# Optimization experiments

Measured on AMD Instinct MI355X. Metric: run time of the kernel, lower is better.

Reference implementation:

```python
import jax, jax.numpy as jnp
import numpy as np

GAMMA = 1.0        # softmin temperature
BANDWIDTH = 0      # 0 => no Sakoe-Chiba band (numba code only skips when 0 < bw < |i-j|)
BIG = 1e30         # finite stand-in for +inf: exp(-BIG/gamma) underflows to exactly 0 in fp32,
                   # reproducing the inf-initialized R/SigR softmin ratios without NaNs
B, N, M = 32, 512, 512


def setup_inputs() -> dict:
    k1, k2 = jax.random.split(jax.random.key(0))
    D = jax.random.uniform(k1, (B, N, M), dtype=jnp.float32)    # pairwise distances (>= 0)
    Sig = jax.random.uniform(k2, (B, N, M), dtype=jnp.float32)  # per-cell uncertainty
    return {"D": D, "Sig": Sig}


def _soft_dtw(D, Sig):
    """uDTW forward DP (compute_softdtw), vectorized over anti-diagonal wavefronts.
    Returns jnp.stack([R[:, N, M], SigR[:, N, M]]) of shape (2, B)."""
    b, n, m = D.shape
    alpha = 1.0 / GAMMA
    # Dp[i, j] == D_new[i, j] = D[i-1, j-1] with zero border (indices 0..N, 0..M)
    Dp = jnp.pad(D, ((0, 0), (1, 0), (1, 0)))
    Sp = jnp.pad(Sig, ((0, 0), (1, 0), (1, 0)))
    iarr = jnp.arange(n + 1)

    def diag(A, d):
        # A[:, i, d - i] for i = 0..N, zero where j out of [0, M]
        j = d - iarr
        vals = A[:, iarr, jnp.clip(j, 0, m)]
        return jnp.where((j >= 0) & (j <= m), vals, 0.0)

    def shift(x, fill):
        # x[:, i-1] (index i-1 along the diagonal buffer)
        return jnp.concatenate([jnp.full((b, 1), fill, x.dtype), x[:, :-1]], axis=1)

    # diagonal buffers indexed by i; diag d=0 holds R[0,0]=0, rest inf(BIG); diag d=1 all inf
    r2 = jnp.full((b, n + 1), BIG, jnp.float32).at[:, 0].set(0.0)
    r1 = jnp.full((b, n + 1), BIG, jnp.float32)
    s2 = jnp.full((b, n + 1), BIG, jnp.float32).at[:, 0].set(0.0)
    s1 = jnp.full((b, n + 1), BIG, jnp.float32)

    def step(carry, d):
        r2, r1, s2, s1 = carry  # R/SigR diagonals d-2 and d-1
        j = d - iarr
        valid = (iarr >= 1) & (j >= 1) & (j <= m)
        if BANDWIDTH > 0:
            valid = valid & (jnp.abs(iarr - j) <= BANDWIDTH)
        # softmin ratios from R neighbors: (i-1,j-1)=prev2 shifted, (i-1,j)=prev1 shifted, (i,j-1)=prev1
        rr0 = -alpha * shift(r2, BIG)
        rr1 = -alpha * shift(r1, BIG)
        rr2 = -alpha * r1
        rmax = jnp.maximum(jnp.maximum(rr0, rr1), rr2)
        e0 = jnp.exp(rr0 - rmax)
        e1 = jnp.exp(rr1 - rmax)
        e2 = jnp.exp(rr2 - rmax)
        inv = 1.0 / (e0 + e1 + e2)
        p0, p1, p2 = e0 * inv, e1 * inv, e2 * inv
        dDd, dD1, dD2 = diag(Dp, d), diag(Dp, d - 1), diag(Dp, d - 2)
        dSd, dS1, dS2 = diag(Sp, d), diag(Sp, d - 1), diag(Sp, d - 2)
        # R[i,j] = D[i-1,j-1] + softmin-weighted avg of D_new neighbors (uDTW recurrence)
        newR = jnp.where(valid, dDd + p0 * shift(dD2, 0.0) + p1 * shift(dD1, 0.0) + p2 * dD1, BIG)
        newS = jnp.where(valid, dSd + p0 * shift(dS2, 0.0) + p1 * shift(dS1, 0.0) + p2 * dS1, BIG)
        return (r1, newR, s1, newS), None

    (_, rlast, _, slast), _ = jax.lax.scan(step, (r2, r1, s2, s1), jnp.arange(2, n + m + 1))
    # last anti-diagonal d = N + M contains cell (N, M) at index i = N
    return jnp.stack([rlast[:, n], slast[:, n]])  # (2, B)


def reference(D, Sig):
    return _soft_dtw(D, Sig)
```

## Files before the change

kernel.cpp:

```cpp
#include <hip/hip_runtime.h>


constexpr int N = 512;
constexpr int M = 512;
constexpr int BATCH = 32;
constexpr int NM = N + M;
constexpr int K = 32;
constexpr int NB = 32;
constexpr int PHASES = NB + 3;
constexpr float NL2E = -1.4426950408889634f;
constexpr float NLN2 = -0.6931471805599453f;
constexpr float EPS  = 1e-30f;

__device__ __forceinline__ float lane_shr1_or(float oldv, float x) {
  return __int_as_float(__builtin_amdgcn_update_dpp(
      __float_as_int(oldv), __float_as_int(x), 0x138, 0xf, 0xf, false));
}
__device__ __forceinline__ int qclamp(int q) {
  return q < 0 ? 0 : (q > 127 ? 127 : q);
}

__global__ __launch_bounds__(256, 1)
void softdtw_fwd(const float* __restrict__ D,
                 const float* __restrict__ Sig,
                 float* __restrict__ out) {
  const int b = blockIdx.x;
  const int t = threadIdx.x;
  const int w = t >> 6;
  const float4* DrowA4 = (const float4*)(D + ((size_t)b * N + 2 * t) * M);
  const float4* DrowB4 = (const float4*)(D + ((size_t)b * N + 2 * t + 1) * M);

  __shared__ float edgeE[4][768];
  __shared__ float edgeD[4][768];
  for (int idx = t; idx < 4 * 768; idx += 256) {
    (&edgeE[0][0])[idx] = 0.f;
    (&edgeD[0][0])[idx] = 0.f;
  }

  float eSelfA = 0.f, dSelfA = 0.f;
  float eA1 = 0.f, dA1 = 0.f;
  float eN2A = (t == 0) ? 1.f : 0.f;
  float dN2A = 0.f;
  float eSelfB = 0.f, dSelfB = 0.f;

  float sgA = 0.f, sg0 = 0.f, sg1 = 0.f, sg2 = 0.f;
  if (t == 255) {
    const float* Sb = Sig + (size_t)b * N * M;
    sgA = Sb[(size_t)(N - 1) * M + (M - 1)];
    sg0 = Sb[(size_t)(N - 2) * M + (M - 2)];
    sg1 = Sb[(size_t)(N - 2) * M + (M - 1)];
    sg2 = Sb[(size_t)(N - 1) * M + (M - 2)];
  }

  const int Bl = 4 * w, Bh = 4 * w + 19;
  const bool sA2 = (t & 1) != 0;
  const bool sB2 = (t & 1) == 0;

  float4 u0,u1,u2,u3,u4,u5,u6,u7,u8;
  float4 v0,v1,v2,v3,v4,v5,v6,v7,v8;
  {
    const int qa = (32 * Bl - 2 * t) >> 2;
    u0 = DrowA4[qclamp(qa + 0)]; u1 = DrowA4[qclamp(qa + 1)];
    u2 = DrowA4[qclamp(qa + 2)]; u3 = DrowA4[qclamp(qa + 3)];
    u4 = DrowA4[qclamp(qa + 4)]; u5 = DrowA4[qclamp(qa + 5)];
    u6 = DrowA4[qclamp(qa + 6)]; u7 = DrowA4[qclamp(qa + 7)];
    u8 = DrowA4[qclamp(qa + 8)];
    const int qb = (32 * Bl - 2 * t - 1) >> 2;
    v0 = DrowB4[qclamp(qb + 0)]; v1 = DrowB4[qclamp(qb + 1)];
    v2 = DrowB4[qclamp(qb + 2)]; v3 = DrowB4[qclamp(qb + 3)];
    v4 = DrowB4[qclamp(qb + 4)]; v5 = DrowB4[qclamp(qb + 5)];
    v6 = DrowB4[qclamp(qb + 6)]; v7 = DrowB4[qclamp(qb + 7)];
    v8 = DrowB4[qclamp(qb + 8)];
  }
  __syncthreads();

  for (int p = 0; p < PHASES; ++p) {
    const int B = p - w;
    const int nB = B + 1;
    const bool dopre = (nB >= Bl) && (nB <= Bh);

    float4 pu0,pu1,pu2,pu3,pu4,pu5,pu6,pu7,pu8;
    float4 pv0,pv1,pv2,pv3,pv4,pv5,pv6,pv7,pv8;
    if (dopre) {
      const int qa = (32 * nB - 2 * t) >> 2;
      pu0 = DrowA4[qclamp(qa + 0)]; pu1 = DrowA4[qclamp(qa + 1)];
      pu2 = DrowA4[qclamp(qa + 2)]; pu3 = DrowA4[qclamp(qa + 3)];
      pu4 = DrowA4[qclamp(qa + 4)]; pu5 = DrowA4[qclamp(qa + 5)];
      pu6 = DrowA4[qclamp(qa + 6)]; pu7 = DrowA4[qclamp(qa + 7)];
      pu8 = DrowA4[qclamp(qa + 8)];
      const int qb = (32 * nB - 2 * t - 1) >> 2;
      pv0 = DrowB4[qclamp(qb + 0)]; pv1 = DrowB4[qclamp(qb + 1)];
      pv2 = DrowB4[qclamp(qb + 2)]; pv3 = DrowB4[qclamp(qb + 3)];
      pv4 = DrowB4[qclamp(qb + 4)]; pv5 = DrowB4[qclamp(qb + 5)];
      pv6 = DrowB4[qclamp(qb + 6)]; pv7 = DrowB4[qclamp(qb + 7)];
      pv8 = DrowB4[qclamp(qb + 8)];
    }

    if (B >= Bl && B <= Bh) {
      const int d0 = 2 + B * K;
      const int cA0 = 32 * B - 2 * t;

      float4 nE0,nE1,nE2,nE3,nE4,nE5,nE6,nE7;
      float4 nD0,nD1,nD2,nD3,nD4,nD5,nD6,nD7;
      if (w > 0) {
        const int ebase = 32 * B - 128 * w + 128;
        const float4* epE = (const float4*)&edgeE[w - 1][ebase];
        const float4* epD = (const float4*)&edgeD[w - 1][ebase];
        nE0 = epE[0]; nE1 = epE[1]; nE2 = epE[2]; nE3 = epE[3];
        nE4 = epE[4]; nE5 = epE[5]; nE6 = epE[6]; nE7 = epE[7];
        nD0 = epD[0]; nD1 = epD[1]; nD2 = epD[2]; nD3 = epD[3];
        nD4 = epD[4]; nD5 = epD[5]; nD6 = epD[6]; nD7 = epD[7];
      } else {
        const float4 z = make_float4(0.f, 0.f, 0.f, 0.f);
        nE0=z;nE1=z;nE2=z;nE3=z;nE4=z;nE5=z;nE6=z;nE7=z;
        nD0=z;nD1=z;nD2=z;nD3=z;nD4=z;nD5=z;nD6=z;nD7=z;
      }

      const float
        A0=u0.x, A1=u0.y, A2=u0.z, A3=u0.w,  A4=u1.x, A5=u1.y, A6=u1.z, A7=u1.w,
        A8=u2.x, A9=u2.y, A10=u2.z, A11=u2.w, A12=u3.x, A13=u3.y, A14=u3.z, A15=u3.w,
        A16=u4.x, A17=u4.y, A18=u4.z, A19=u4.w, A20=u5.x, A21=u5.y, A22=u5.z, A23=u5.w,
        A24=u6.x, A25=u6.y, A26=u6.z, A27=u6.w, A28=u7.x, A29=u7.y, A30=u7.z, A31=u7.w,
        A32=u8.x, A33=u8.y;
      const float
        F1=v0.y, F2=v0.z, F3=v0.w,  F4=v1.x, F5=v1.y, F6=v1.z, F7=v1.w,
        F8=v2.x, F9=v2.y, F10=v2.z, F11=v2.w, F12=v3.x, F13=v3.y, F14=v3.z, F15=v3.w,
        F16=v4.x, F17=v4.y, F18=v4.z, F19=v4.w, F20=v5.x, F21=v5.y, F22=v5.z, F23=v5.w,
        F24=v6.x, F25=v6.y, F26=v6.z, F27=v6.w, F28=v7.x, F29=v7.y, F30=v7.z, F31=v7.w,
        F32=v8.x, F33=v8.y, F34=v8.z;

      const float
        gA0 =sA2?A2 :A0,  gA1 =sA2?A3 :A1,  gA2 =sA2?A4 :A2,  gA3 =sA2?A5 :A3,
        gA4 =sA2?A6 :A4,  gA5 =sA2?A7 :A5,  gA6 =sA2?A8 :A6,  gA7 =sA2?A9 :A7,
        gA8 =sA2?A10:A8,  gA9 =sA2?A11:A9,  gA10=sA2?A12:A10, gA11=sA2?A13:A11,
        gA12=sA2?A14:A12, gA13=sA2?A15:A13, gA14=sA2?A16:A14, gA15=sA2?A17:A15,
        gA16=sA2?A18:A16, gA17=sA2?A19:A17, gA18=sA2?A20:A18, gA19=sA2?A21:A19,
        gA20=sA2?A22:A20, gA21=sA2?A23:A21, gA22=sA2?A24:A22, gA23=sA2?A25:A23,
        gA24=sA2?A26:A24, gA25=sA2?A27:A25, gA26=sA2?A28:A26, gA27=sA2?A29:A27,
        gA28=sA2?A30:A28, gA29=sA2?A31:A29, gA30=sA2?A32:A30, gA31=sA2?A33:A31;
      const float
        gB0 =sB2?F3 :F1,  gB1 =sB2?F4 :F2,  gB2 =sB2?F5 :F3,  gB3 =sB2?F6 :F4,
        gB4 =sB2?F7 :F5,  gB5 =sB2?F8 :F6,  gB6 =sB2?F9 :F7,  gB7 =sB2?F10:F8,
        gB8 =sB2?F11:F9,  gB9 =sB2?F12:F10, gB10=sB2?F13:F11, gB11=sB2?F14:F12,
        gB12=sB2?F15:F13, gB13=sB2?F16:F14, gB14=sB2?F17:F15, gB15=sB2?F18:F16,
        gB16=sB2?F19:F17, gB17=sB2?F20:F18, gB18=sB2?F21:F19, gB19=sB2?F22:F20,
        gB20=sB2?F23:F21, gB21=sB2?F24:F22, gB22=sB2?F25:F23, gB23=sB2?F26:F24,
        gB24=sB2?F27:F25, gB25=sB2?F28:F26, gB26=sB2?F29:F27, gB27=sB2?F30:F28,
        gB28=sB2?F31:F29, gB29=sB2?F32:F30, gB30=sB2?F33:F31, gB31=sB2?F34:F32;

      float* pE = &edgeE[w][128 + cA0 - 1];
      float* pD = &edgeD[w][128 + cA0 - 1];

#define STEP(kk, NEv, NDv, GA, GB)                                            \
      {                                                                       \
        const float eA0v = eSelfA, dA0v = dSelfA;                             \
        const float eB0v = eSelfB, dB0v = dSelfB;                             \
        const int cA = cA0 + (kk);                                            \
        const float ddLA = (GA) * NL2E;                                       \
        const float ddLAm = ((unsigned)cA < 512u) ? ddLA : -1e30f;            \
        const float ddLB = (GB) * NL2E;                                       \
        const float ddLBm = ((unsigned)(cA - 1) < 512u) ? ddLB : -1e30f;      \
        const float sEA = lane_shr1_or((NEv), eB0v);                          \
        const float sDA = lane_shr1_or((NDv), dB0v);                          \
        const float sumA = ((eN2A + eA0v) + EPS) + sEA;                       \
        const float invA = __builtin_amdgcn_rcpf(sumA);                       \
        const float numA = fmaf(eN2A, dN2A, fmaf(sEA, sDA, eA0v * dA0v));     \
        const float rrA = fmaf(invA, numA, ddLAm);                            \
        const float newEA = __builtin_amdgcn_exp2f(rrA);                      \
        const float sumB = ((eA1 + eB0v) + EPS) + eA0v;                       \
        const float invB = __builtin_amdgcn_rcpf(sumB);                       \
        const float numB = fmaf(eA1, dA1, fmaf(eA0v, dA0v, eB0v * dB0v));     \
        const float rrB = fmaf(invB, numB, ddLBm);                            \
        const float newEB = __builtin_amdgcn_exp2f(rrB);                      \
        if (d0 + (kk) == NM && t == 255) {                                    \
          out[b] = rrB * NLN2;                                                \
          out[BATCH + b] = sgA + invB * (eA1 * sg0 + eA0v * sg1 + eB0v * sg2);\
        }                                                                     \
        eN2A = sEA; dN2A = sDA;                                               \
        eA1 = eA0v; dA1 = dA0v;                                               \
        eSelfA = newEA; dSelfA = ddLA;                                        \
        eSelfB = newEB; dSelfB = ddLB;                                        \
        pE[kk] = newEB;                                                       \
        pD[kk] = ddLB;                                                        \
      }

      STEP(0,  nE0.x, nD0.x, gA0,  gB0)
      STEP(1,  nE0.y, nD0.y, gA1,  gB1)
      STEP(2,  nE0.z, nD0.z, gA2,  gB2)
      STEP(3,  nE0.w, nD0.w, gA3,  gB3)
      STEP(4,  nE1.x, nD1.x, gA4,  gB4)
      STEP(5,  nE1.y, nD1.y, gA5,  gB5)
      STEP(6,  nE1.z, nD1.z, gA6,  gB6)
      STEP(7,  nE1.w, nD1.w, gA7,  gB7)
      STEP(8,  nE2.x, nD2.x, gA8,  gB8)
      STEP(9,  nE2.y, nD2.y, gA9,  gB9)
      STEP(10, nE2.z, nD2.z, gA10, gB10)
      STEP(11, nE2.w, nD2.w, gA11, gB11)
      STEP(12, nE3.x, nD3.x, gA12, gB12)
      STEP(13, nE3.y, nD3.y, gA13, gB13)
      STEP(14, nE3.z, nD3.z, gA14, gB14)
      STEP(15, nE3.w, nD3.w, gA15, gB15)
      STEP(16, nE4.x, nD4.x, gA16, gB16)
      STEP(17, nE4.y, nD4.y, gA17, gB17)
      STEP(18, nE4.z, nD4.z, gA18, gB18)
      STEP(19, nE4.w, nD4.w, gA19, gB19)
      STEP(20, nE5.x, nD5.x, gA20, gB20)
      STEP(21, nE5.y, nD5.y, gA21, gB21)
      STEP(22, nE5.z, nD5.z, gA22, gB22)
      STEP(23, nE5.w, nD5.w, gA23, gB23)
      STEP(24, nE6.x, nD6.x, gA24, gB24)
      STEP(25, nE6.y, nD6.y, gA25, gB25)
      STEP(26, nE6.z, nD6.z, gA26, gB26)
      STEP(27, nE6.w, nD6.w, gA27, gB27)
      STEP(28, nE7.x, nD7.x, gA28, gB28)
      STEP(29, nE7.y, nD7.y, gA29, gB29)
      STEP(30, nE7.z, nD7.z, gA30, gB30)
      STEP(31, nE7.w, nD7.w, gA31, gB31)
#undef STEP
    }

    if (dopre) {
      u0 = pu0; u1 = pu1; u2 = pu2; u3 = pu3; u4 = pu4;
      u5 = pu5; u6 = pu6; u7 = pu7; u8 = pu8;
      v0 = pv0; v1 = pv1; v2 = pv2; v3 = pv3; v4 = pv4;
      v5 = pv5; v6 = pv6; v7 = pv7; v8 = pv8;
    }
    __syncthreads();
  }
}

extern "C" void kernel_launch(void* const* d_in, const int* in_sizes, int n_in,
                              void* d_out, int out_size, void* d_ws, size_t ws_size,
                              hipStream_t stream) {
  const float* D   = (const float*)d_in[0];
  const float* Sig = (const float*)d_in[1];
  float* out = (float*)d_out;
  softdtw_fwd<<<dim3(BATCH), dim3(256), 0, stream>>>(D, Sig, out);
}
```

Measured before the change: 202.8 us.

## Pack two batches per block and split edge buffers by parity

```diff
diff --git a/kernel.cpp b/kernel.cpp
--- a/kernel.cpp
+++ b/kernel.cpp
@@ -20,31 +20,39 @@
   return q < 0 ? 0 : (q > 127 ? 127 : q);
 }
 
-__global__ __launch_bounds__(256, 1)
+__global__ __launch_bounds__(512, 1)
 void softdtw_fwd(const float* __restrict__ D,
                  const float* __restrict__ Sig,
                  float* __restrict__ out) {
-  const int b = blockIdx.x;
-  const int t = threadIdx.x;
-  const int w = t >> 6;
-  const float4* DrowA4 = (const float4*)(D + ((size_t)b * N + 2 * t) * M);
-  const float4* DrowB4 = (const float4*)(D + ((size_t)b * N + 2 * t + 1) * M);
-
-  __shared__ float edgeE[4][768];
-  __shared__ float edgeD[4][768];
-  for (int idx = t; idx < 4 * 768; idx += 256) {
-    (&edgeE[0][0])[idx] = 0.f;
-    (&edgeD[0][0])[idx] = 0.f;
+  const int t  = threadIdx.x;
+  const int h  = t >> 8;
+  const int tl = t & 255;
+  const int w  = tl >> 6;
+  const int b  = 2 * blockIdx.x + h;
+
+  const float4* DrowA4 = (const float4*)(D + ((size_t)b * N + 2 * tl) * M);
+  const float4* DrowB4 = (const float4*)(D + ((size_t)b * N + 2 * tl + 1) * M);
+
+  __shared__ float eOdd [2][4][384];
+  __shared__ float eEven[2][4][384];
+  __shared__ float dOdd [2][4][384];
+  __shared__ float dEven[2][4][384];
+  {
+    float* z0 = &eOdd[0][0][0];  float* z1 = &eEven[0][0][0];
+    float* z2 = &dOdd[0][0][0];  float* z3 = &dEven[0][0][0];
+    for (int idx = t; idx < 2 * 4 * 384; idx += 512) {
+      z0[idx] = 0.f; z1[idx] = 0.f; z2[idx] = 0.f; z3[idx] = 0.f;
+    }
   }
 
   float eSelfA = 0.f, dSelfA = 0.f;
   float eA1 = 0.f, dA1 = 0.f;
-  float eN2A = (t == 0) ? 1.f : 0.f;
+  float eN2A = (tl == 0) ? 1.f : 0.f;
   float dN2A = 0.f;
   float eSelfB = 0.f, dSelfB = 0.f;
 
   float sgA = 0.f, sg0 = 0.f, sg1 = 0.f, sg2 = 0.f;
-  if (t == 255) {
+  if (tl == 255) {
     const float* Sb = Sig + (size_t)b * N * M;
     sgA = Sb[(size_t)(N - 1) * M + (M - 1)];
     sg0 = Sb[(size_t)(N - 2) * M + (M - 2)];
@@ -53,19 +61,19 @@
   }
 
   const int Bl = 4 * w, Bh = 4 * w + 19;
-  const bool sA2 = (t & 1) != 0;
-  const bool sB2 = (t & 1) == 0;
+  const bool sA2 = (tl & 1) != 0;
+  const bool sB2 = (tl & 1) == 0;
 
   float4 u0,u1,u2,u3,u4,u5,u6,u7,u8;
   float4 v0,v1,v2,v3,v4,v5,v6,v7,v8;
   {
-    const int qa = (32 * Bl - 2 * t) >> 2;
+    const int qa = (32 * Bl - 2 * tl) >> 2;
     u0 = DrowA4[qclamp(qa + 0)]; u1 = DrowA4[qclamp(qa + 1)];
     u2 = DrowA4[qclamp(qa + 2)]; u3 = DrowA4[qclamp(qa + 3)];
     u4 = DrowA4[qclamp(qa + 4)]; u5 = DrowA4[qclamp(qa + 5)];
     u6 = DrowA4[qclamp(qa + 6)]; u7 = DrowA4[qclamp(qa + 7)];
     u8 = DrowA4[qclamp(qa + 8)];
-    const int qb = (32 * Bl - 2 * t - 1) >> 2;
+    const int qb = (32 * Bl - 2 * tl - 1) >> 2;
     v0 = DrowB4[qclamp(qb + 0)]; v1 = DrowB4[qclamp(qb + 1)];
     v2 = DrowB4[qclamp(qb + 2)]; v3 = DrowB4[qclamp(qb + 3)];
     v4 = DrowB4[qclamp(qb + 4)]; v5 = DrowB4[qclamp(qb + 5)];
@@ -82,13 +90,13 @@
     float4 pu0,pu1,pu2,pu3,pu4,pu5,pu6,pu7,pu8;
     float4 pv0,pv1,pv2,pv3,pv4,pv5,pv6,pv7,pv8;
     if (dopre) {
-      const int qa = (32 * nB - 2 * t) >> 2;
+      const int qa = (32 * nB - 2 * tl) >> 2;
       pu0 = DrowA4[qclamp(qa + 0)]; pu1 = DrowA4[qclamp(qa + 1)];
       pu2 = DrowA4[qclamp(qa + 2)]; pu3 = DrowA4[qclamp(qa + 3)];
       pu4 = DrowA4[qclamp(qa + 4)]; pu5 = DrowA4[qclamp(qa + 5)];
       pu6 = DrowA4[qclamp(qa + 6)]; pu7 = DrowA4[qclamp(qa + 7)];
       pu8 = DrowA4[qclamp(qa + 8)];
-      const int qb = (32 * nB - 2 * t - 1) >> 2;
+      const int qb = (32 * nB - 2 * tl - 1) >> 2;
       pv0 = DrowB4[qclamp(qb + 0)]; pv1 = DrowB4[qclamp(qb + 1)];
       pv2 = DrowB4[qclamp(qb + 2)]; pv3 = DrowB4[qclamp(qb + 3)];
       pv4 = DrowB4[qclamp(qb + 4)]; pv5 = DrowB4[qclamp(qb + 5)];
@@ -98,22 +106,24 @@
 
     if (B >= Bl && B <= Bh) {
       const int d0 = 2 + B * K;
-      const int cA0 = 32 * B - 2 * t;
-
-      float4 nE0,nE1,nE2,nE3,nE4,nE5,nE6,nE7;
-      float4 nD0,nD1,nD2,nD3,nD4,nD5,nD6,nD7;
+      const int cA0 = 32 * B - 2 * tl;
+
+      float4 mEe0,mEe1,mEe2,mEe3, mEo0,mEo1,mEo2,mEo3;
+      float4 mDe0,mDe1,mDe2,mDe3, mDo0,mDo1,mDo2,mDo3;
       if (w > 0) {
-        const int ebase = 32 * B - 128 * w + 128;
-        const float4* epE = (const float4*)&edgeE[w - 1][ebase];
-        const float4* epD = (const float4*)&edgeD[w - 1][ebase];
-        nE0 = epE[0]; nE1 = epE[1]; nE2 = epE[2]; nE3 = epE[3];
-        nE4 = epE[4]; nE5 = epE[5]; nE6 = epE[6]; nE7 = epE[7];
-        nD0 = epD[0]; nD1 = epD[1]; nD2 = epD[2]; nD3 = epD[3];
-        nD4 = epD[4]; nD5 = epD[5]; nD6 = epD[6]; nD7 = epD[7];
+        const int hb = 16 * B - 64 * w + 64;
+        const float4* pe = (const float4*)&eEven[h][w - 1][hb];
+        const float4* po = (const float4*)&eOdd [h][w - 1][hb];
+        const float4* qe = (const float4*)&dEven[h][w - 1][hb];
+        const float4* qo = (const float4*)&dOdd [h][w - 1][hb];
+        mEe0 = pe[0]; mEe1 = pe[1]; mEe2 = pe[2]; mEe3 = pe[3];
+        mEo0 = po[0]; mEo1 = po[1]; mEo2 = po[2]; mEo3 = po[3];
+        mDe0 = qe[0]; mDe1 = qe[1]; mDe2 = qe[2]; mDe3 = qe[3];
+        mDo0 = qo[0]; mDo1 = qo[1]; mDo2 = qo[2]; mDo3 = qo[3];
       } else {
         const float4 z = make_float4(0.f, 0.f, 0.f, 0.f);
-        nE0=z;nE1=z;nE2=z;nE3=z;nE4=z;nE5=z;nE6=z;nE7=z;
-        nD0=z;nD1=z;nD2=z;nD3=z;nD4=z;nD5=z;nD6=z;nD7=z;
+        mEe0=z;mEe1=z;mEe2=z;mEe3=z; mEo0=z;mEo1=z;mEo2=z;mEo3=z;
+        mDe0=z;mDe1=z;mDe2=z;mDe3=z; mDo0=z;mDo1=z;mDo2=z;mDo3=z;
       }
 
       const float
@@ -148,10 +158,13 @@
         gB24=sB2?F27:F25, gB25=sB2?F28:F26, gB26=sB2?F29:F27, gB27=sB2?F30:F28,
         gB28=sB2?F31:F29, gB29=sB2?F32:F30, gB30=sB2?F33:F31, gB31=sB2?F34:F32;
 
-      float* pE = &edgeE[w][128 + cA0 - 1];
-      float* pD = &edgeD[w][128 + cA0 - 1];
-
-#define STEP(kk, NEv, NDv, GA, GB)                                            \
+      const int sb = 16 * B - tl;
+      float* pEo = &eOdd [h][w][63 + sb];
+      float* pEe = &eEven[h][w][64 + sb];
+      float* pDo = &dOdd [h][w][63 + sb];
+      float* pDe = &dEven[h][w][64 + sb];
+
+#define STEP(kk, NEv, NDv, GA, GB, PE_, PD_, ix)                              \
       {                                                                       \
         const float eA0v = eSelfA, dA0v = dSelfA;                             \
         const float eB0v = eSelfB, dB0v = dSelfB;                             \
@@ -172,7 +185,7 @@
         const float numB = fmaf(eA1, dA1, fmaf(eA0v, dA0v, eB0v * dB0v));     \
         const float rrB = fmaf(invB, numB, ddLBm);                            \
         const float newEB = __builtin_amdgcn_exp2f(rrB);                      \
-        if (d0 + (kk) == NM && t == 255) {                                    \
+        if (d0 + (kk) == NM && tl == 255) {                                   \
           out[b] = rrB * NLN2;                                                \
           out[BATCH + b] = sgA + invB * (eA1 * sg0 + eA0v * sg1 + eB0v * sg2);\
         }                                                                     \
@@ -180,42 +193,42 @@
         eA1 = eA0v; dA1 = dA0v;                                               \
         eSelfA = newEA; dSelfA = ddLA;                                        \
         eSelfB = newEB; dSelfB = ddLB;                                        \
-        pE[kk] = newEB;                                                       \
-        pD[kk] = ddLB;                                                        \
+        PE_[ix] = newEB;                                                      \
+        PD_[ix] = ddLB;                                                       \
       }
 
-      STEP(0,  nE0.x, nD0.x, gA0,  gB0)
-      STEP(1,  nE0.y, nD0.y, gA1,  gB1)
-      STEP(2,  nE0.z, nD0.z, gA2,  gB2)
-      STEP(3,  nE0.w, nD0.w, gA3,  gB3)
-      STEP(4,  nE1.x, nD1.x, gA4,  gB4)
-      STEP(5,  nE1.y, nD1.y, gA5,  gB5)
-      STEP(6,  nE1.z, nD1.z, gA6,  gB6)
-      STEP(7,  nE1.w, nD1.w, gA7,  gB7)
-      STEP(8,  nE2.x, nD2.x, gA8,  gB8)
-      STEP(9,  nE2.y, nD2.y, gA9,  gB9)
-      STEP(10, nE2.z, nD2.z, gA10, gB10)
-      STEP(11, nE2.w, nD2.w, gA11, gB11)
-      STEP(12, nE3.x, nD3.x, gA12, gB12)
-      STEP(13, nE3.y, nD3.y, gA13, gB13)
-      STEP(14, nE3.z, nD3.z, gA14, gB14)
-      STEP(15, nE3.w, nD3.w, gA15, gB15)
-      STEP(16, nE4.x, nD4.x, gA16, gB16)
-      STEP(17, nE4.y, nD4.y, gA17, gB17)
-      STEP(18, nE4.z, nD4.z, gA18, gB18)
-      STEP(19, nE4.w, nD4.w, gA19, gB19)
-      STEP(20, nE5.x, nD5.x, gA20, gB20)
-      STEP(21, nE5.y, nD5.y, gA21, gB21)
-      STEP(22, nE5.z, nD5.z, gA22, gB22)
-      STEP(23, nE5.w, nD5.w, gA23, gB23)
-      STEP(24, nE6.x, nD6.x, gA24, gB24)
-      STEP(25, nE6.y, nD6.y, gA25, gB25)
-      STEP(26, nE6.z, nD6.z, gA26, gB26)
-      STEP(27, nE6.w, nD6.w, gA27, gB27)
-      STEP(28, nE7.x, nD7.x, gA28, gB28)
-      STEP(29, nE7.y, nD7.y, gA29, gB29)
-      STEP(30, nE7.z, nD7.z, gA30, gB30)
-      STEP(31, nE7.w, nD7.w, gA31, gB31)
+      STEP(0,  mEe0.x, mDe0.x, gA0,  gB0,  pEo, pDo, 0)
+      STEP(1,  mEo0.x, mDo0.x, gA1,  gB1,  pEe, pDe, 0)
+      STEP(2,  mEe0.y, mDe0.y, gA2,  gB2,  pEo, pDo, 1)
+      STEP(3,  mEo0.y, mDo0.y, gA3,  gB3,  pEe, pDe, 1)
+      STEP(4,  mEe0.z, mDe0.z, gA4,  gB4,  pEo, pDo, 2)
+      STEP(5,  mEo0.z, mDo0.z, gA5,  gB5,  pEe, pDe, 2)
+      STEP(6,  mEe0.w, mDe0.w, gA6,  gB6,  pEo, pDo, 3)
+      STEP(7,  mEo0.w, mDo0.w, gA7,  gB7,  pEe, pDe, 3)
+      STEP(8,  mEe1.x, mDe1.x, gA8,  gB8,  pEo, pDo, 4)
+      STEP(9,  mEo1.x, mDo1.x, gA9,  gB9,  pEe, pDe, 4)
+      STEP(10, mEe1.y, mDe1.y, gA10, gB10, pEo, pDo, 5)
+      STEP(11, mEo1.y, mDo1.y, gA11, gB11, pEe, pDe, 5)
+      STEP(12, mEe1.z, mDe1.z, gA12, gB12, pEo, pDo, 6)
+      STEP(13, mEo1.z, mDo1.z, gA13, gB13, pEe, pDe, 6)
+      STEP(14, mEe1.w, mDe1.w, gA14, gB14, pEo, pDo, 7)
+      STEP(15, mEo1.w, mDo1.w, gA15, gB15, pEe, pDe, 7)
+      STEP(16, mEe2.x, mDe2.x, gA16, gB16, pEo, pDo, 8)
+      STEP(17, mEo2.x, mDo2.x, gA17, gB17, pEe, pDe, 8)
+      STEP(18, mEe2.y, mDe2.y, gA18, gB18, pEo, pDo, 9)
+      STEP(19, mEo2.y, mDo2.y, gA19, gB19, pEe, pDe, 9)
+      STEP(20, mEe2.z, mDe2.z, gA20, gB20, pEo, pDo, 10)
+      STEP(21, mEo2.z, mDo2.z, gA21, gB21, pEe, pDe, 10)
+      STEP(22, mEe2.w, mDe2.w, gA22, gB22, pEo, pDo, 11)
+      STEP(23, mEo2.w, mDo2.w, gA23, gB23, pEe, pDe, 11)
+      STEP(24, mEe3.x, mDe3.x, gA24, gB24, pEo, pDo, 12)
+      STEP(25, mEo3.x, mDo3.x, gA25, gB25, pEe, pDe, 12)
+      STEP(26, mEe3.y, mDe3.y, gA26, gB26, pEo, pDo, 13)
+      STEP(27, mEo3.y, mDo3.y, gA27, gB27, pEe, pDe, 13)
+      STEP(28, mEe3.z, mDe3.z, gA28, gB28, pEo, pDo, 14)
+      STEP(29, mEo3.z, mDo3.z, gA29, gB29, pEe, pDe, 14)
+      STEP(30, mEe3.w, mDe3.w, gA30, gB30, pEo, pDo, 15)
+      STEP(31, mEo3.w, mDo3.w, gA31, gB31, pEe, pDe, 15)
 #undef STEP
     }
 
@@ -235,5 +248,5 @@
   const float* D   = (const float*)d_in[0];
   const float* Sig = (const float*)d_in[1];
   float* out = (float*)d_out;
-  softdtw_fwd<<<dim3(BATCH), dim3(256), 0, stream>>>(D, Sig, out);
-}
+  softdtw_fwd<<<dim3(BATCH / 2), dim3(512), 0, stream>>>(D, Sig, out);
+}
```

Result: slower. 486.9 us (+140.1%).
